# Optimization experiments

Measured on AMD Instinct MI355X. Metric: run time of the kernel, lower is better.

The kernel has to match this reference:

```python
import jax, jax.numpy as jnp
import numpy as np


def _gru(x, Wih, Whh, bih, bhh):
    # single-layer torch-style GRU; x: [B,T,D] -> [B,T,H]
    H = Whh.shape[1]
    gi_all = jnp.einsum('btd,gd->btg', x, Wih) + bih  # [B,T,3H], input gates precomputed

    def step(h, gi):
        gh = h @ Whh.T + bhh
        ir, iz, inn = jnp.split(gi, 3, axis=-1)
        hr, hz, hn = jnp.split(gh, 3, axis=-1)
        r = jax.nn.sigmoid(ir + hr)
        zg = jax.nn.sigmoid(iz + hz)
        n = jnp.tanh(inn + r * hn)
        h_new = (1.0 - zg) * n + zg * h
        return h_new, h_new

    h0 = jnp.zeros((x.shape[0], H), x.dtype)
    _, hs = jax.lax.scan(step, h0, jnp.swapaxes(gi_all, 0, 1))
    return jnp.swapaxes(hs, 0, 1)


def _post(h, W1, b1, W2, b2):
    h = jax.nn.leaky_relu(h @ W1.T + b1, 0.1)
    return jax.nn.leaky_relu(h @ W2.T + b2, 0.1)


def setup_inputs() -> dict:
    B, T, X, Z, H, L = 512, 100, 38, 3, 500, 20
    key = jax.random.key(0)
    ks = iter(jax.random.split(key, 40))
    r = lambda shape, s=0.05: jax.random.normal(next(ks), shape, jnp.float32) * s
    return {
        'x': jax.random.normal(next(ks), (B, T, X), jnp.float32),
        'eps': jax.random.normal(next(ks), (B, T, Z), jnp.float32),
        'enc_Wih': r((3 * H, X)), 'enc_Whh': r((3 * H, H)), 'enc_bih': r((3 * H,)), 'enc_bhh': r((3 * H,)),
        'enc_W1': r((H, H)), 'enc_b1': r((H,)), 'enc_W2': r((H, H)), 'enc_b2': r((H,)),
        'zm_W': r((Z, H + Z)), 'zm_b': r((Z,)), 'zs_W': r((Z, H + Z)), 'zs_b': r((Z,)),
        'flow_w': r((L, Z), 0.5), 'flow_b': r((L,), 0.5), 'flow_u': r((L, Z), 0.5),
        'dec_Wih': r((3 * H, Z)), 'dec_Whh': r((3 * H, H)), 'dec_bih': r((3 * H,)), 'dec_bhh': r((3 * H,)),
        'dec_W1': r((H, H)), 'dec_b1': r((H,)), 'dec_W2': r((H, H)), 'dec_b2': r((H,)),
        'xm_W': r((X, H)), 'xm_b': r((X,)), 'xs_W': r((X, H)), 'xs_b': r((X,)),
    }


def reference(x, eps, enc_Wih, enc_Whh, enc_bih, enc_bhh, enc_W1, enc_b1, enc_W2, enc_b2,
              zm_W, zm_b, zs_W, zs_b, flow_w, flow_b, flow_u,
              dec_Wih, dec_Whh, dec_bih, dec_bhh, dec_W1, dec_b1, dec_W2, dec_b2,
              xm_W, xm_b, xs_W, xs_b):
    # ---- Encoder ----
    h = _gru(x, enc_Wih, enc_Whh, enc_bih, enc_bhh)
    h = _post(h, enc_W1, enc_b1, enc_W2, enc_b2)

    def lat_step(z_prev, inputs):
        ht, et = inputs
        inp = jnp.concatenate([ht, z_prev], axis=-1)
        mu = inp @ zm_W.T + zm_b
        std = jax.nn.softplus(inp @ zs_W.T + zs_b) + 1e-4
        zt = mu + std * et
        return zt, (zt, mu, std)

    z0 = jnp.zeros((x.shape[0], zm_W.shape[0]), x.dtype)
    _, (z_gen, z_mu, z_std) = jax.lax.scan(
        lat_step, z0, (jnp.swapaxes(h, 0, 1), jnp.swapaxes(eps, 0, 1)))
    z_gen = jnp.swapaxes(z_gen, 0, 1)
    z_mu = jnp.swapaxes(z_mu, 0, 1)
    z_std = jnp.swapaxes(z_std, 0, 1)

    # ---- Planar flow stack ----
    def flow_step(carry, p):
        z, ld = carry
        w, b, u = p
        wu = jnp.sum(w * u)
        m = -1.0 + jax.nn.softplus(wu)
        u_hat = u + (m - wu) * w / (jnp.sum(w * w) + 1e-7)
        lin = jnp.sum(z * w, axis=-1, keepdims=True) + b  # [B,T,1]
        t = jnp.tanh(lin)
        fz = z + u_hat * t
        det = 1.0 + (1.0 - t * t) * jnp.sum(u_hat * w)  # sum(u_hat*psi)
        ld = ld + jnp.log(jnp.abs(det) + 1e-7)
        return (fz, ld), None

    ld0 = jnp.zeros(z_gen.shape[:-1] + (1,), z_gen.dtype)
    (z_fin, log_det_jac), _ = jax.lax.scan(flow_step, (z_gen, ld0), (flow_w, flow_b, flow_u))

    # ---- Decoder ----
    hd = _gru(z_fin, dec_Wih, dec_Whh, dec_bih, dec_bhh)
    hd = _post(hd, dec_W1, dec_b1, dec_W2, dec_b2)
    x_rec_mu = hd @ xm_W.T + xm_b
    x_rec_std = jax.nn.softplus(hd @ xs_W.T + xs_b) + 1e-4
    return (x_rec_mu, x_rec_std, z_gen, z_fin, z_mu, z_std, log_det_jac)
```

## Files before the change

### kernel.cpp

```cpp
#include <hip/hip_runtime.h>

typedef unsigned short u16;
typedef unsigned int u32;
typedef unsigned long long u64;
typedef __bf16 bf16x8 __attribute__((ext_vector_type(8)));
typedef float f32x4 __attribute__((ext_vector_type(4)));
typedef u16 u16x8 __attribute__((ext_vector_type(8)));
typedef u16 u16x4 __attribute__((ext_vector_type(4)));
typedef u32 u32x4 __attribute__((ext_vector_type(4)));

#define MFMA16x16(a,b,c) __builtin_amdgcn_mfma_f32_16x16x32_bf16((a),(b),(c),0,0,0)

static __device__ __forceinline__ u16 f2bf(float f){
  u32 u = __builtin_bit_cast(u32, f);
  u += 0x7fffu + ((u >> 16) & 1u);
  return (u16)(u >> 16);
}
static __device__ __forceinline__ float bf2f(u16 h){
  u32 u = ((u32)h) << 16;
  return __builtin_bit_cast(float, u);
}
static __device__ __forceinline__ float fast_sigmoid(float x){
  return 1.f / (1.f + __expf(-x));
}
static __device__ __forceinline__ float fast_tanh(float x){
  float e = __expf(2.f * x);
  return 1.f - 2.f / (e + 1.f);
}
static __device__ __forceinline__ float fast_softplus(float x){
  return (x > 15.f) ? x : __logf(1.f + __expf(x));
}
static __device__ __forceinline__ f32x4 zero4(){
  f32x4 v; v[0]=0.f; v[1]=0.f; v[2]=0.f; v[3]=0.f; return v;
}
static __device__ __forceinline__ f32x4 splat4(float x){
  f32x4 v; v[0]=x; v[1]=x; v[2]=x; v[3]=x; return v;
}

static __device__ __forceinline__ void build_one(
    u16* __restrict__ dst, int mode, int NT, int idx,
    const float* __restrict__ W0, const float* __restrict__ b0,
    const float* __restrict__ W1, const float* __restrict__ b1)
{
  int j    = idx & 7;
  int lane = (idx >> 3) & 63;
  int ntks = idx >> 9;
  int nt   = ntks % NT;
  int ks   = ntks / NT;
  int k    = ks * 32 + ((lane >> 4) << 3) + j;
  int ncol = (nt << 4) + (lane & 15);
  float v = 0.f;
  if (mode == 0){
    int g = ncol >> 9;
    int jin = ncol & 511;
    if (jin < 500){
      int row = g * 500 + jin;
      if (k < 500) v = W0[row * 500 + k];
      else if (k == 511) v = b0[row];
    }
  } else if (mode == 2){
    if (ncol < 500){
      if (k < 500) v = W0[ncol * 500 + k];
      else if (k == 511) v = b0[ncol];
    }
  } else if (mode == 3){
    int c = ncol;
    if (c < 3){
      if (k < 500) v = W0[c * 503 + k];
      else if (k == 511) v = b0[c];
    } else if (c < 6){
      int cc = c - 3;
      if (k < 500) v = W1[cc * 503 + k];
      else if (k == 511) v = b1[cc];
    }
  } else if (mode == 4){
    int grp = ncol / 48;
    int cc  = ncol - grp * 48;
    if (grp < 2 && cc < 38){
      const float* W  = grp ? W1 : W0;
      const float* bb = grp ? b1 : b0;
      if (k < 500) v = W[cc * 500 + k];
      else if (k == 511) v = bb[cc];
    }
  } else {
    int g = ncol >> 9;
    int jin = ncol & 511;
    if (jin < 500 && k < 38) v = W0[(g * 500 + jin) * 38 + k];
  }
  dst[idx] = f2bf(v);
}

__global__ void build_all(
    u16* ENCF, u16* DECF, u16* EGIF, u16* PF0, u16* PF1, u16* PF2, u16* PF3,
    u16* ZFR, u16* HFR, float* FPP, u32* CNT,
    const float* enc_Whh, const float* enc_bhh, const float* enc_Wih,
    const float* dec_Whh, const float* dec_bhh,
    const float* enc_W1, const float* enc_b1, const float* enc_W2, const float* enc_b2,
    const float* dec_W1, const float* dec_b1, const float* dec_W2, const float* dec_b2,
    const float* zm_W, const float* zm_b, const float* zs_W, const float* zs_b,
    const float* xm_W, const float* xm_b, const float* xs_W, const float* xs_b,
    const float* flow_w, const float* flow_b, const float* flow_u)
{
  const int b = blockIdx.x, tid = threadIdx.x;
  if      (b < 3072)  build_one(ENCF,0,96,(b       )*256+tid, enc_Whh,enc_bhh,0,0);
  else if (b < 6144)  build_one(DECF,0,96,(b- 3072 )*256+tid, dec_Whh,dec_bhh,0,0);
  else if (b < 6528)  build_one(EGIF,5,96,(b- 6144 )*256+tid, enc_Wih,0,0,0);
  else if (b < 7552)  build_one(PF0 ,2,32,(b- 6528 )*256+tid, enc_W1,enc_b1,0,0);
  else if (b < 8576)  build_one(PF1 ,2,32,(b- 7552 )*256+tid, enc_W2,enc_b2,0,0);
  else if (b < 9600)  build_one(PF2 ,2,32,(b- 8576 )*256+tid, dec_W1,dec_b1,0,0);
  else if (b < 10624) build_one(PF3 ,2,32,(b- 9600 )*256+tid, dec_W2,dec_b2,0,0);
  else if (b < 10656) build_one(ZFR ,3, 1,(b-10624 )*256+tid, zm_W,zm_b,zs_W,zs_b);
  else if (b < 10848) build_one(HFR ,4, 6,(b-10656 )*256+tid, xm_W,xm_b,xs_W,xs_b);
  else if (b == 10848){
    if (tid < 20){
      int l = tid;
      float w0 = flow_w[l*3+0], w1 = flow_w[l*3+1], w2 = flow_w[l*3+2];
      float u0 = flow_u[l*3+0], u1 = flow_u[l*3+1], u2 = flow_u[l*3+2];
      float wu = w0*u0 + w1*u1 + w2*u2;
      float m  = -1.f + fast_softplus(wu);
      float ww = w0*w0 + w1*w1 + w2*w2 + 1e-7f;
      float sc = (m - wu) / ww;
      float uh0 = u0 + sc*w0, uh1 = u1 + sc*w1, uh2 = u2 + sc*w2;
      float uw  = uh0*w0 + uh1*w1 + uh2*w2;
      FPP[l*8+0]=w0; FPP[l*8+1]=w1; FPP[l*8+2]=w2; FPP[l*8+3]=flow_b[l];
      FPP[l*8+4]=uh0; FPP[l*8+5]=uh1; FPP[l*8+6]=uh2; FPP[l*8+7]=uw;
    }
  } else {
    for (int i = tid; i < 8192; i += 256) CNT[i] = 0;
  }
}

__global__ __launch_bounds__(256, 1) void gru8_kernel(
    const u16* __restrict__ frag, const u16* __restrict__ giw,
    const float* __restrict__ xsrc, const u64* __restrict__ zsrc,
    const float* __restrict__ Wih3, const float* __restrict__ bih3,
    u32* __restrict__ hbufbase, u16* __restrict__ hout, u32* __restrict__ cntbase)
{
  __shared__ u32 hstage[20800];
  __shared__ u16 xstage[1280];
  const int tid  = threadIdx.x, lane = tid & 63;
  const int wv   = tid >> 6;
  const int q    = lane >> 4, c = lane & 15;
  const int gid  = blockIdx.x & 31, s = blockIdx.x >> 5;
  const int b0   = gid * 16;
  const int nt0  = s*4 + wv;
  const int col  = nt0*16 + c;
  u32* cnt = cntbase + gid * 128;
  u32* hb  = hbufbase + (size_t)gid * 8192;
  const bool enc = (giw != nullptr);

  u16x8 wf[3][16];
  #pragma unroll
  for (int ks = 0; ks < 16; ++ks)
    #pragma unroll
    for (int g = 0; g < 3; ++g)
      wf[g][ks] = *(const u16x8*)(frag + (((size_t)ks*96 + g*32 + nt0)*64 + lane)*8);

  u16x8 wih[2][3];
  float bs0 = 0.f, bs1 = 0.f, bs2 = 0.f;
  int xr0=0, xk0=0, xr1=0, xk1=0, xr2=0, xk2=0;
  if (enc){
    #pragma unroll
    for (int ks = 0; ks < 2; ++ks)
      #pragma unroll
      for (int g = 0; g < 3; ++g)
        wih[ks][g] = *(const u16x8*)(giw + (((size_t)ks*96 + g*32 + nt0)*64 + lane)*8);
    if (col < 500){
      bs0 = bih3[col]; bs1 = bih3[500 + col]; bs2 = bih3[1000 + col];
    }
    xr0 = tid / 38;         xk0 = tid - xr0*38;
    int e1 = tid + 256;     xr1 = e1 / 38; xk1 = e1 - xr1*38;
    if (tid < 96){ int e2 = tid + 512; xr2 = e2 / 38; xk2 = e2 - xr2*38; }
  }

  float wz[3][3] = {{0,0,0},{0,0,0},{0,0,0}}, wb[3] = {0,0,0};
  if (!enc && col < 500){
    #pragma unroll
    for (int g = 0; g < 3; ++g){
      #pragma unroll
      for (int k = 0; k < 3; ++k) wz[g][k] = Wih3[(g*500 + col)*3 + k];
      wb[g] = bih3[g*500 + col];
    }
  }

  const int srow = tid >> 4;
  const int spos = (tid & 15) * 2;

  float hold[4] = {0.f, 0.f, 0.f, 0.f};
  u64 zv[4];
  float xf0 = 0.f, xf1 = 0.f, xf2 = 0.f;
  {
    u32 me = (col == 511) ? 0x3F80u : 0u;
    u32 pr = __shfl_xor(me, 1, 64);
    if (!(c & 1)){
      u32 val = me | (pr << 16);
      #pragma unroll
      for (int r = 0; r < 4; ++r){
        hstage[(q*4+r)*260 + (col>>1)] = val;
        __hip_atomic_store(hb + (q*4+r)*256 + (col>>1), val,
                           __ATOMIC_RELAXED, __HIP_MEMORY_SCOPE_AGENT);
      }
    }
    if (enc){
      if (tid < 64){
        int slot = tid >> 5, r = tid & 15, p = (tid >> 4) & 1;
        xstage[slot*640 + r*40 + 38 + p] = 0;
      }
      float v0 = xsrc[((size_t)(b0 + xr0)*100 + 0)*38 + xk0];
      float v1 = xsrc[((size_t)(b0 + xr1)*100 + 0)*38 + xk1];
      xstage[xr0*40 + xk0] = f2bf(v0);
      xstage[xr1*40 + xk1] = f2bf(v1);
      if (tid < 96){
        float v2 = xsrc[((size_t)(b0 + xr2)*100 + 0)*38 + xk2];
        xstage[xr2*40 + xk2] = f2bf(v2);
      }
    } else {
      #pragma unroll
      for (int r = 0; r < 4; ++r)
        zv[r] = zsrc[(size_t)(b0 + q*4 + r)*100 + 0];
    }
  }
  __syncthreads();
  if (tid == 0)
    __hip_atomic_fetch_add(cnt, 1u, __ATOMIC_RELAXED, __HIP_MEMORY_SCOPE_AGENT);

  #pragma unroll 1
  for (int t = 0; t < 100; ++t){
    if (tid == 0){
      const u32 target = 8u*(u32)(t+1);
      int guard = 0;
      while (__hip_atomic_load(cnt, __ATOMIC_RELAXED, __HIP_MEMORY_SCOPE_AGENT) < target){
        if (++guard > (1<<24)) break;
      }
    }
    __syncthreads();

    {
      const u64* src = (const u64*)(hb + (t & 1)*4096);
      u64 sv[7];
      #pragma unroll
      for (int r = 0; r < 7; ++r){
        const int rs = (s + 1 + r) & 7;
        sv[r] = __hip_atomic_load(src + srow*128 + rs*16 + (tid & 15),
                                  __ATOMIC_RELAXED, __HIP_MEMORY_SCOPE_AGENT);
      }
      if (enc && t < 99){
        xf0 = xsrc[((size_t)(b0 + xr0)*100 + (t+1))*38 + xk0];
        xf1 = xsrc[((size_t)(b0 + xr1)*100 + (t+1))*38 + xk1];
        if (tid < 96) xf2 = xsrc[((size_t)(b0 + xr2)*100 + (t+1))*38 + xk2];
      }
      #pragma unroll
      for (int r = 0; r < 7; ++r){
        const int rs = (s + 1 + r) & 7;
        *(u64*)&hstage[srow*260 + rs*32 + spos] = sv[r];
      }
    }
    __syncthreads();

    f32x4 acc0, acc1, acc2, gN;
    if (enc){
      const int slot = t & 1;
      bf16x8 ax0 = *(const bf16x8*)&xstage[slot*640 + c*40 + q*8];
      u16x8 z8 = {0,0,0,0,0,0,0,0};
      bf16x8 ax1 = __builtin_bit_cast(bf16x8, z8);
      if (q == 0) ax1 = *(const bf16x8*)&xstage[slot*640 + c*40 + 32];
      acc0 = splat4(bs0);
      acc0 = MFMA16x16(ax0, __builtin_bit_cast(bf16x8, wih[0][0]), acc0);
      acc0 = MFMA16x16(ax1, __builtin_bit_cast(bf16x8, wih[1][0]), acc0);
      acc1 = splat4(bs1);
      acc1 = MFMA16x16(ax0, __builtin_bit_cast(bf16x8, wih[0][1]), acc1);
      acc1 = MFMA16x16(ax1, __builtin_bit_cast(bf16x8, wih[1][1]), acc1);
      gN   = splat4(bs2);
      gN   = MFMA16x16(ax0, __builtin_bit_cast(bf16x8, wih[0][2]), gN);
      gN   = MFMA16x16(ax1, __builtin_bit_cast(bf16x8, wih[1][2]), gN);
      acc2 = zero4();
    } else {
      acc0 = zero4(); acc1 = zero4(); acc2 = zero4(); gN = zero4();
    }
    #pragma unroll
    for (int ks = 0; ks < 16; ++ks){
      bf16x8 af = *(const bf16x8*)&hstage[c*260 + ks*16 + q*4];
      acc0 = MFMA16x16(af, __builtin_bit_cast(bf16x8, wf[0][ks]), acc0);
      acc1 = MFMA16x16(af, __builtin_bit_cast(bf16x8, wf[1][ks]), acc1);
      acc2 = MFMA16x16(af, __builtin_bit_cast(bf16x8, wf[2][ks]), acc2);
    }
    __syncthreads();

    if (enc && t < 99){
      const int ns = (t+1) & 1;
      xstage[ns*640 + xr0*40 + xk0] = f2bf(xf0);
      xstage[ns*640 + xr1*40 + xk1] = f2bf(xf1);
      if (tid < 96) xstage[ns*640 + xr2*40 + xk2] = f2bf(xf2);
    }

    u16 hvv[4];
    u32* nxt = hb + ((t+1) & 1)*4096;
    {
      #pragma unroll
      for (int r = 0; r < 4; ++r){
        float ar, az, gn;
        if (enc){
          ar = acc0[r]; az = acc1[r]; gn = gN[r];
        } else {
          float z0 = bf2f((u16)(zv[r]));
          float z1 = bf2f((u16)(zv[r] >> 16));
          float z2 = bf2f((u16)(zv[r] >> 32));
          ar = acc0[r] + z0*wz[0][0] + z1*wz[0][1] + z2*wz[0][2] + wb[0];
          az = acc1[r] + z0*wz[1][0] + z1*wz[1][1] + z2*wz[1][2] + wb[1];
          gn = z0*wz[2][0] + z1*wz[2][1] + z2*wz[2][2] + wb[2];
        }
        float an = acc2[r];
        float rr = fast_sigmoid(ar);
        float zz = fast_sigmoid(az);
        float nn = fast_tanh(gn + rr*an);
        float h  = (1.f - zz)*nn + zz*hold[r];
        hold[r] = h;
        u16 hv16 = (col < 500) ? f2bf(h) : ((col == 511) ? (u16)0x3F80 : (u16)0);
        hvv[r] = hv16;
        u32 me = hv16;
        u32 pr = __shfl_xor(me, 1, 64);
        if (!(c & 1)){
          u32 val = me | (pr << 16);
          hstage[(q*4+r)*260 + (col>>1)] = val;
          __hip_atomic_store(nxt + (q*4+r)*256 + (col>>1), val,
                             __ATOMIC_RELAXED, __HIP_MEMORY_SCOPE_AGENT);
        }
      }
    }
    __syncthreads();
    if (tid == 0)
      __hip_atomic_fetch_add(cnt, 1u, __ATOMIC_RELAXED, __HIP_MEMORY_SCOPE_AGENT);
    #pragma unroll
    for (int r = 0; r < 4; ++r)
      __builtin_nontemporal_store(hvv[r],
          hout + ((size_t)(b0 + q*4 + r)*100 + t)*512 + col);
    if (!enc && t < 99){
      #pragma unroll
      for (int r = 0; r < 4; ++r)
        zv[r] = zsrc[(size_t)(b0 + q*4 + r)*100 + (t+1)];
    }
  }
}

__global__ __launch_bounds__(512, 4) void post_chain(
    const u16* __restrict__ A, const u16* __restrict__ fA,
    const u16* __restrict__ fB, const u16* __restrict__ f3,
    float* __restrict__ o0, float* __restrict__ o1, int mode)
{
  __shared__ u16 AS[32768];
  const int tid = threadIdx.x, lane = tid & 63, w = tid >> 6;
  const int q = lane >> 4, c = lane & 15;
  const size_t rowbase = (size_t)blockIdx.x * 64;

  f32x4 acc[4][4];
  #pragma unroll
  for (int rt = 0; rt < 4; ++rt)
    #pragma unroll
    for (int i = 0; i < 4; ++i) acc[rt][i] = zero4();
  #pragma unroll 1
  for (int ks = 0; ks < 16; ++ks){
    bf16x8 bfr[4];
    #pragma unroll
    for (int i = 0; i < 4; ++i){
      const int nt = w*4 + i;
      bfr[i] = __builtin_bit_cast(bf16x8,
          *(const u16x8*)(fA + (((size_t)ks * 32 + nt) * 64 + lane) * 8));
    }
    #pragma unroll
    for (int rt = 0; rt < 4; ++rt){
      bf16x8 af = __builtin_bit_cast(bf16x8,
          *(const u16x8*)(A + (rowbase + rt*16 + c) * 512 + ks * 32 + q * 8));
      #pragma unroll
      for (int i = 0; i < 4; ++i)
        acc[rt][i] = MFMA16x16(af, bfr[i], acc[rt][i]);
    }
  }
  #pragma unroll
  for (int rt = 0; rt < 4; ++rt)
    #pragma unroll
    for (int i = 0; i < 4; ++i){
      const int cl = (w*4 + i)*16 + c;
      const int ks2 = cl >> 5, qq = (cl >> 3) & 3, j = cl & 7;
      #pragma unroll
      for (int r = 0; r < 4; ++r){
        const int m = q*4 + r;
        float v = acc[rt][i][r];
        v = fmaxf(v, 0.1f * v);
        AS[(((rt*16 + ks2)*4 + qq)*16 + m)*8 + j] =
            (cl < 500) ? f2bf(v) : ((cl == 511) ? (u16)0x3F80 : (u16)0);
      }
    }
  __syncthreads();

  #pragma unroll
  for (int rt = 0; rt < 4; ++rt)
    #pragma unroll
    for (int i = 0; i < 4; ++i) acc[rt][i] = zero4();
  #pragma unroll 1
  for (int ks = 0; ks < 16; ++ks){
    bf16x8 bfr[4];
    #pragma unroll
    for (int i = 0; i < 4; ++i){
      const int nt = w*4 + i;
      bfr[i] = __builtin_bit_cast(bf16x8,
          *(const u16x8*)(fB + (((size_t)ks * 32 + nt) * 64 + lane) * 8));
    }
    #pragma unroll
    for (int rt = 0; rt < 4; ++rt){
      bf16x8 af = __builtin_bit_cast(bf16x8,
          *(const u16x8*)&AS[(((rt*16 + ks)*4 + q)*16 + c)*8]);
      #pragma unroll
      for (int i = 0; i < 4; ++i)
        acc[rt][i] = MFMA16x16(af, bfr[i], acc[rt][i]);
    }
  }
  __syncthreads();
  #pragma unroll
  for (int rt = 0; rt < 4; ++rt)
    #pragma unroll
    for (int i = 0; i < 4; ++i){
      const int cl = (w*4 + i)*16 + c;
      const int ks2 = cl >> 5, qq = (cl >> 3) & 3, j = cl & 7;
      #pragma unroll
      for (int r = 0; r < 4; ++r){
        const int m = q*4 + r;
        float v = acc[rt][i][r];
        v = fmaxf(v, 0.1f * v);
        AS[(((rt*16 + ks2)*4 + qq)*16 + m)*8 + j] =
            (cl < 500) ? f2bf(v) : ((cl == 511) ? (u16)0x3F80 : (u16)0);
      }
    }
  __syncthreads();

  if (mode == 0){
    if (w < 4){
      const int rt3 = w;
      f32x4 a3 = zero4();
      #pragma unroll 1
      for (int ks = 0; ks < 16; ++ks){
        bf16x8 af = __builtin_bit_cast(bf16x8,
            *(const u16x8*)&AS[(((rt3*16 + ks)*4 + q)*16 + c)*8]);
        bf16x8 bf = __builtin_bit_cast(bf16x8,
            *(const u16x8*)(f3 + (((size_t)ks * 64) + lane) * 8));
        a3 = MFMA16x16(af, bf, a3);
      }
      if (c < 6){
        #pragma unroll
        for (int r = 0; r < 4; ++r){
          const size_t row = rowbase + rt3*16 + q*4 + r;
          const int tt = (int)(row % 100);
          const int bb = (int)(row / 100);
          o0[((size_t)tt*512 + bb)*8 + c] = a3[r];
        }
      }
    }
  } else {
    const int rt3 = w & 3, hh = w >> 2;
    f32x4 a3[3];
    #pragma unroll
    for (int ii = 0; ii < 3; ++ii) a3[ii] = zero4();
    #pragma unroll 1
    for (int ks = 0; ks < 16; ++ks){
      bf16x8 af = __builtin_bit_cast(bf16x8,
          *(const u16x8*)&AS[(((rt3*16 + ks)*4 + q)*16 + c)*8]);
      #pragma unroll
      for (int ii = 0; ii < 3; ++ii){
        const int nt = hh*3 + ii;
        bf16x8 bf = __builtin_bit_cast(bf16x8,
            *(const u16x8*)(f3 + (((size_t)ks * 6 + nt) * 64 + lane) * 8));
        a3[ii] = MFMA16x16(af, bf, a3[ii]);
      }
    }
    #pragma unroll
    for (int ii = 0; ii < 3; ++ii){
      const int cc = (hh*3 + ii)*16 + c;
      const int grp = cc / 48;
      const int cl = cc - grp * 48;
      if (cl < 38){
        #pragma unroll
        for (int r = 0; r < 4; ++r){
          const size_t row = rowbase + rt3*16 + q*4 + r;
          if (grp == 0) o0[row*38 + cl] = a3[ii][r];
          else          o1[row*38 + cl] = fast_softplus(a3[ii][r]) + 1e-4f;
        }
      }
    }
  }
}

__global__ void scan_kernel(const float* __restrict__ hmT, const float* __restrict__ eps,
                            const float* __restrict__ zmW, const float* __restrict__ zsW,
                            float* __restrict__ zgen, float* __restrict__ zmu,
                            float* __restrict__ zstd)
{
  int b = blockIdx.x * blockDim.x + threadIdx.x;
  if (b >= 512) return;
  float Wm[3][3], Ws[3][3];
  #pragma unroll
  for (int j = 0; j < 3; ++j)
    #pragma unroll
    for (int k = 0; k < 3; ++k){
      Wm[j][k] = zmW[j * 503 + 500 + k];
      Ws[j][k] = zsW[j * 503 + 500 + k];
    }
  f32x4 hA0, hA1, hB0, hB1;
  float eA0, eA1, eA2, eB0, eB1, eB2;
  hA0 = *(const f32x4*)(hmT + ((size_t)0*512 + b)*8);
  hA1 = *(const f32x4*)(hmT + ((size_t)0*512 + b)*8 + 4);
  hB0 = *(const f32x4*)(hmT + ((size_t)1*512 + b)*8);
  hB1 = *(const f32x4*)(hmT + ((size_t)1*512 + b)*8 + 4);
  {
    const float* e0p = eps + ((size_t)b*100 + 0)*3;
    const float* e1p = eps + ((size_t)b*100 + 1)*3;
    eA0 = e0p[0]; eA1 = e0p[1]; eA2 = e0p[2];
    eB0 = e1p[0]; eB1 = e1p[1]; eB2 = e1p[2];
  }
  float z0 = 0.f, z1 = 0.f, z2 = 0.f;
  #pragma unroll 1
  for (int t = 0; t < 100; t += 2){
    {
      float h0 = hA0[0], h1 = hA0[1], h2 = hA0[2];
      float h3 = hA0[3], h4 = hA1[0], h5 = hA1[1];
      float e0 = eA0, e1 = eA1, e2 = eA2;
      if (t + 2 < 100){
        hA0 = *(const f32x4*)(hmT + ((size_t)(t+2)*512 + b)*8);
        hA1 = *(const f32x4*)(hmT + ((size_t)(t+2)*512 + b)*8 + 4);
        const float* ep = eps + ((size_t)b*100 + (t+2))*3;
        eA0 = ep[0]; eA1 = ep[1]; eA2 = ep[2];
      }
      size_t row = (size_t)b*100 + t;
      float m0 = h0 + Wm[0][0]*z0 + Wm[0][1]*z1 + Wm[0][2]*z2;
      float m1 = h1 + Wm[1][0]*z0 + Wm[1][1]*z1 + Wm[1][2]*z2;
      float m2 = h2 + Wm[2][0]*z0 + Wm[2][1]*z1 + Wm[2][2]*z2;
      float s0 = fast_softplus(h3 + Ws[0][0]*z0 + Ws[0][1]*z1 + Ws[0][2]*z2) + 1e-4f;
      float s1 = fast_softplus(h4 + Ws[1][0]*z0 + Ws[1][1]*z1 + Ws[1][2]*z2) + 1e-4f;
      float s2 = fast_softplus(h5 + Ws[2][0]*z0 + Ws[2][1]*z1 + Ws[2][2]*z2) + 1e-4f;
      z0 = m0 + s0*e0; z1 = m1 + s1*e1; z2 = m2 + s2*e2;
      __builtin_nontemporal_store(z0, zgen + row*3 + 0);
      __builtin_nontemporal_store(z1, zgen + row*3 + 1);
      __builtin_nontemporal_store(z2, zgen + row*3 + 2);
      __builtin_nontemporal_store(m0, zmu  + row*3 + 0);
      __builtin_nontemporal_store(m1, zmu  + row*3 + 1);
      __builtin_nontemporal_store(m2, zmu  + row*3 + 2);
      __builtin_nontemporal_store(s0, zstd + row*3 + 0);
      __builtin_nontemporal_store(s1, zstd + row*3 + 1);
      __builtin_nontemporal_store(s2, zstd + row*3 + 2);
    }
    {
      float h0 = hB0[0], h1 = hB0[1], h2 = hB0[2];
      float h3 = hB0[3], h4 = hB1[0], h5 = hB1[1];
      float e0 = eB0, e1 = eB1, e2 = eB2;
      if (t + 3 < 100){
        hB0 = *(const f32x4*)(hmT + ((size_t)(t+3)*512 + b)*8);
        hB1 = *(const f32x4*)(hmT + ((size_t)(t+3)*512 + b)*8 + 4);
        const float* ep = eps + ((size_t)b*100 + (t+3))*3;
        eB0 = ep[0]; eB1 = ep[1]; eB2 = ep[2];
      }
      size_t row = (size_t)b*100 + t + 1;
      float m0 = h0 + Wm[0][0]*z0 + Wm[0][1]*z1 + Wm[0][2]*z2;
      float m1 = h1 + Wm[1][0]*z0 + Wm[1][1]*z1 + Wm[1][2]*z2;
      float m2 = h2 + Wm[2][0]*z0 + Wm[2][1]*z1 + Wm[2][2]*z2;
      float s0 = fast_softplus(h3 + Ws[0][0]*z0 + Ws[0][1]*z1 + Ws[0][2]*z2) + 1e-4f;
      float s1 = fast_softplus(h4 + Ws[1][0]*z0 + Ws[1][1]*z1 + Ws[1][2]*z2) + 1e-4f;
      float s2 = fast_softplus(h5 + Ws[2][0]*z0 + Ws[2][1]*z1 + Ws[2][2]*z2) + 1e-4f;
      z0 = m0 + s0*e0; z1 = m1 + s1*e1; z2 = m2 + s2*e2;
      __builtin_nontemporal_store(z0, zgen + row*3 + 0);
      __builtin_nontemporal_store(z1, zgen + row*3 + 1);
      __builtin_nontemporal_store(z2, zgen + row*3 + 2);
      __builtin_nontemporal_store(m0, zmu  + row*3 + 0);
      __builtin_nontemporal_store(m1, zmu  + row*3 + 1);
      __builtin_nontemporal_store(m2, zmu  + row*3 + 2);
      __builtin_nontemporal_store(s0, zstd + row*3 + 0);
      __builtin_nontemporal_store(s1, zstd + row*3 + 1);
      __builtin_nontemporal_store(s2, zstd + row*3 + 2);
    }
  }
}

__global__ void flow_kernel(const float* __restrict__ zgen, const float* __restrict__ fp,
                            float* __restrict__ zfin, float* __restrict__ ldj,
                            u16* __restrict__ zf16)
{
  int idx = blockIdx.x * blockDim.x + threadIdx.x;
  if (idx >= 51200) return;
  float z0 = zgen[idx*3+0], z1 = zgen[idx*3+1], z2 = zgen[idx*3+2];
  float ld = 0.f;
  #pragma unroll 1
  for (int l = 0; l < 20; ++l){
    const float* p = fp + l * 8;
    float lin = z0*p[0] + z1*p[1] + z2*p[2] + p[3];
    float tt = fast_tanh(lin);
    z0 += p[4]*tt; z1 += p[5]*tt; z2 += p[6]*tt;
    float det = 1.f + (1.f - tt*tt) * p[7];
    ld += __logf(fabsf(det) + 1e-7f);
  }
  zfin[idx*3+0] = z0; zfin[idx*3+1] = z1; zfin[idx*3+2] = z2;
  ldj[idx] = ld;
  u16x4 o; o[0] = f2bf(z0); o[1] = f2bf(z1); o[2] = f2bf(z2); o[3] = 0x3F80;
  *(u16x4*)(zf16 + (size_t)idx * 4) = o;
}

extern "C" void kernel_launch(void* const* d_in, const int* in_sizes, int n_in,
                              void* d_out, int out_size, void* d_ws, size_t ws_size,
                              hipStream_t stream)
{
  const float* x       = (const float*)d_in[0];
  const float* eps     = (const float*)d_in[1];
  const float* enc_Wih = (const float*)d_in[2];
  const float* enc_Whh = (const float*)d_in[3];
  const float* enc_bih = (const float*)d_in[4];
  const float* enc_bhh = (const float*)d_in[5];
  const float* enc_W1  = (const float*)d_in[6];
  const float* enc_b1  = (const float*)d_in[7];
  const float* enc_W2  = (const float*)d_in[8];
  const float* enc_b2  = (const float*)d_in[9];
  const float* zm_W    = (const float*)d_in[10];
  const float* zm_b    = (const float*)d_in[11];
  const float* zs_W    = (const float*)d_in[12];
  const float* zs_b    = (const float*)d_in[13];
  const float* flow_w  = (const float*)d_in[14];
  const float* flow_b  = (const float*)d_in[15];
  const float* flow_u  = (const float*)d_in[16];
  const float* dec_Wih = (const float*)d_in[17];
  const float* dec_Whh = (const float*)d_in[18];
  const float* dec_bih = (const float*)d_in[19];
  const float* dec_bhh = (const float*)d_in[20];
  const float* dec_W1  = (const float*)d_in[21];
  const float* dec_b1  = (const float*)d_in[22];
  const float* dec_W2  = (const float*)d_in[23];
  const float* dec_b2  = (const float*)d_in[24];
  const float* xm_W    = (const float*)d_in[25];
  const float* xm_b    = (const float*)d_in[26];
  const float* xs_W    = (const float*)d_in[27];
  const float* xs_b    = (const float*)d_in[28];
  (void)in_sizes; (void)n_in; (void)out_size; (void)ws_size;

  float* out    = (float*)d_out;
  float* r_mu   = out;
  float* r_std  = out + 1945600;
  float* r_zgen = out + 3891200;
  float* r_zfin = out + 4044800;
  float* r_zmu  = out + 4198400;
  float* r_zstd = out + 4352000;
  float* r_ldj  = out + 4505600;

  char* ws = (char*)d_ws;
  size_t off = 0;
  auto alloc = [&](size_t bytes)->char*{
    char* p = ws + off;
    off += (bytes + 255) & ~(size_t)255;
    return p;
  };
  u16* H1    = (u16*)alloc((size_t)51200*512*2);
  u16* ENCF  = (u16*)alloc((size_t)16*96*512*2);
  u16* DECF  = (u16*)alloc((size_t)16*96*512*2);
  u16* EGIF  = (u16*)alloc((size_t)2*96*512*2);
  u16* PF0   = (u16*)alloc((size_t)16*32*512*2);
  u16* PF1   = (u16*)alloc((size_t)16*32*512*2);
  u16* PF2   = (u16*)alloc((size_t)16*32*512*2);
  u16* PF3   = (u16*)alloc((size_t)16*32*512*2);
  u16* ZFR   = (u16*)alloc((size_t)16*1*512*2);
  u16* HFR   = (u16*)alloc((size_t)16*6*512*2);
  float* FPP = (float*)alloc((size_t)20*8*4);
  float* HM  = (float*)alloc((size_t)51200*8*4);
  u16* ZF16  = (u16*)alloc((size_t)51200*4*2);
  u32* HBUF  = (u32*)alloc((size_t)32*2*16*512*2);
  u32* CNT   = (u32*)alloc((size_t)2*32*128*4);

  build_all<<<10850,256,0,stream>>>(ENCF,DECF,EGIF,PF0,PF1,PF2,PF3,ZFR,HFR,FPP,CNT,
      enc_Whh,enc_bhh,enc_Wih,dec_Whh,dec_bhh,
      enc_W1,enc_b1,enc_W2,enc_b2,dec_W1,dec_b1,dec_W2,dec_b2,
      zm_W,zm_b,zs_W,zs_b,xm_W,xm_b,xs_W,xs_b,flow_w,flow_b,flow_u);

  gru8_kernel<<<256,256,0,stream>>>(ENCF, EGIF, x, nullptr, nullptr, enc_bih,
                                    HBUF, H1, CNT);
  post_chain<<<800,512,0,stream>>>(H1, PF0, PF1, ZFR, HM, nullptr, 0);

  scan_kernel<<<2,256,0,stream>>>(HM, eps, zm_W, zs_W, r_zgen, r_zmu, r_zstd);
  flow_kernel<<<200,256,0,stream>>>(r_zgen, FPP, r_zfin, r_ldj, ZF16);

  gru8_kernel<<<256,256,0,stream>>>(DECF, nullptr, nullptr, (const u64*)ZF16,
                                    dec_Wih, dec_bih, HBUF, H1, CNT + 32*128);
  post_chain<<<800,512,0,stream>>>(H1, PF2, PF3, HFR, r_mu, r_std, 1);
}
```

Before: 1.035 ms.

## Split GRU recurrent K-reduction across two wave halves with LDS partial-sum combine

Doubles the GRU block to 512 threads and splits the 16-step K loop of the recurrent matmul between two wave groups, each holding half the Whh fragments. The upper half also computes the input-gate MFMAs and writes its partial accumulators to shared memory, where the lower half adds them before applying the gate nonlinearities. The goal is a shorter per-timestep critical path on the serial recurrence and fewer weight registers per wave. The cost is an extra LDS round trip and two waves per SIMD competing for issue slots, and all waves still wait at every barrier.

Result: slower. 1.138 ms (+9.9%).

```diff
diff --git a/kernel.cpp b/kernel.cpp
--- a/kernel.cpp
+++ b/kernel.cpp
@@ -130,7 +130,7 @@
   }
 }
 
-__global__ __launch_bounds__(256, 1) void gru8_kernel(
+__global__ __launch_bounds__(512, 2) void gru8_kernel(
     const u16* __restrict__ frag, const u16* __restrict__ giw,
     const float* __restrict__ xsrc, const u64* __restrict__ zsrc,
     const float* __restrict__ Wih3, const float* __restrict__ bih3,
@@ -138,28 +138,32 @@
 {
   __shared__ u32 hstage[20800];
   __shared__ u16 xstage[1280];
+  __shared__ f32x4 pacc[4][64][4];
   const int tid  = threadIdx.x, lane = tid & 63;
-  const int wv   = tid >> 6;
+  const int wv8  = tid >> 6;
+  const int half = wv8 & 1;
+  const int wq   = wv8 >> 1;
   const int q    = lane >> 4, c = lane & 15;
   const int gid  = blockIdx.x & 31, s = blockIdx.x >> 5;
   const int b0   = gid * 16;
-  const int nt0  = s*4 + wv;
+  const int nt0  = s*4 + wq;
   const int col  = nt0*16 + c;
   u32* cnt = cntbase + gid * 128;
   u32* hb  = hbufbase + (size_t)gid * 8192;
   const bool enc = (giw != nullptr);
 
-  u16x8 wf[3][16];
+  u16x8 wf[3][8];
   #pragma unroll
-  for (int ks = 0; ks < 16; ++ks)
+  for (int ksl = 0; ksl < 8; ++ksl){
+    const int ks = half*8 + ksl;
     #pragma unroll
     for (int g = 0; g < 3; ++g)
-      wf[g][ks] = *(const u16x8*)(frag + (((size_t)ks*96 + g*32 + nt0)*64 + lane)*8);
+      wf[g][ksl] = *(const u16x8*)(frag + (((size_t)ks*96 + g*32 + nt0)*64 + lane)*8);
+  }
 
   u16x8 wih[2][3];
   float bs0 = 0.f, bs1 = 0.f, bs2 = 0.f;
-  int xr0=0, xk0=0, xr1=0, xk1=0, xr2=0, xk2=0;
-  if (enc){
+  if (enc && half == 1){
     #pragma unroll
     for (int ks = 0; ks < 2; ++ks)
       #pragma unroll
@@ -168,13 +172,17 @@
     if (col < 500){
       bs0 = bih3[col]; bs1 = bih3[500 + col]; bs2 = bih3[1000 + col];
     }
+  }
+
+  int xr0=0, xk0=0, xr1=0, xk1=0, xr2=0, xk2=0;
+  if (enc && tid < 256){
     xr0 = tid / 38;         xk0 = tid - xr0*38;
     int e1 = tid + 256;     xr1 = e1 / 38; xk1 = e1 - xr1*38;
     if (tid < 96){ int e2 = tid + 512; xr2 = e2 / 38; xk2 = e2 - xr2*38; }
   }
 
   float wz[3][3] = {{0,0,0},{0,0,0},{0,0,0}}, wb[3] = {0,0,0};
-  if (!enc && col < 500){
+  if (!enc && half == 0 && col < 500){
     #pragma unroll
     for (int g = 0; g < 3; ++g){
       #pragma unroll
@@ -190,15 +198,17 @@
   u64 zv[4];
   float xf0 = 0.f, xf1 = 0.f, xf2 = 0.f;
   {
-    u32 me = (col == 511) ? 0x3F80u : 0u;
-    u32 pr = __shfl_xor(me, 1, 64);
-    if (!(c & 1)){
-      u32 val = me | (pr << 16);
-      #pragma unroll
-      for (int r = 0; r < 4; ++r){
-        hstage[(q*4+r)*260 + (col>>1)] = val;
-        __hip_atomic_store(hb + (q*4+r)*256 + (col>>1), val,
-                           __ATOMIC_RELAXED, __HIP_MEMORY_SCOPE_AGENT);
+    if (half == 0){
+      u32 me = (col == 511) ? 0x3F80u : 0u;
+      u32 pr = __shfl_xor(me, 1, 64);
+      if (!(c & 1)){
+        u32 val = me | (pr << 16);
+        #pragma unroll
+        for (int r = 0; r < 4; ++r){
+          hstage[(q*4+r)*260 + (col>>1)] = val;
+          __hip_atomic_store(hb + (q*4+r)*256 + (col>>1), val,
+                             __ATOMIC_RELAXED, __HIP_MEMORY_SCOPE_AGENT);
+        }
       }
     }
     if (enc){
@@ -206,15 +216,17 @@
         int slot = tid >> 5, r = tid & 15, p = (tid >> 4) & 1;
         xstage[slot*640 + r*40 + 38 + p] = 0;
       }
-      float v0 = xsrc[((size_t)(b0 + xr0)*100 + 0)*38 + xk0];
-      float v1 = xsrc[((size_t)(b0 + xr1)*100 + 0)*38 + xk1];
-      xstage[xr0*40 + xk0] = f2bf(v0);
-      xstage[xr1*40 + xk1] = f2bf(v1);
-      if (tid < 96){
-        float v2 = xsrc[((size_t)(b0 + xr2)*100 + 0)*38 + xk2];
-        xstage[xr2*40 + xk2] = f2bf(v2);
-      }
-    } else {
+      if (tid < 256){
+        float v0 = xsrc[((size_t)(b0 + xr0)*100 + 0)*38 + xk0];
+        float v1 = xsrc[((size_t)(b0 + xr1)*100 + 0)*38 + xk1];
+        xstage[xr0*40 + xk0] = f2bf(v0);
+        xstage[xr1*40 + xk1] = f2bf(v1);
+        if (tid < 96){
+          float v2 = xsrc[((size_t)(b0 + xr2)*100 + 0)*38 + xk2];
+          xstage[xr2*40 + xk2] = f2bf(v2);
+        }
+      }
+    } else if (half == 0){
       #pragma unroll
       for (int r = 0; r < 4; ++r)
         zv[r] = zsrc[(size_t)(b0 + q*4 + r)*100 + 0];
@@ -235,7 +247,7 @@
     }
     __syncthreads();
 
-    {
+    if (tid < 256){
       const u64* src = (const u64*)(hb + (t & 1)*4096);
       u64 sv[7];
       #pragma unroll
@@ -258,7 +270,7 @@
     __syncthreads();
 
     f32x4 acc0, acc1, acc2, gN;
-    if (enc){
+    if (enc && half == 1){
       const int slot = t & 1;
       bf16x8 ax0 = *(const bf16x8*)&xstage[slot*640 + c*40 + q*8];
       u16x8 z8 = {0,0,0,0,0,0,0,0};
@@ -278,24 +290,27 @@
       acc0 = zero4(); acc1 = zero4(); acc2 = zero4(); gN = zero4();
     }
     #pragma unroll
-    for (int ks = 0; ks < 16; ++ks){
-      bf16x8 af = *(const bf16x8*)&hstage[c*260 + ks*16 + q*4];
-      acc0 = MFMA16x16(af, __builtin_bit_cast(bf16x8, wf[0][ks]), acc0);
-      acc1 = MFMA16x16(af, __builtin_bit_cast(bf16x8, wf[1][ks]), acc1);
-      acc2 = MFMA16x16(af, __builtin_bit_cast(bf16x8, wf[2][ks]), acc2);
+    for (int ksl = 0; ksl < 8; ++ksl){
+      bf16x8 af = *(const bf16x8*)&hstage[c*260 + (half*8 + ksl)*16 + q*4];
+      acc0 = MFMA16x16(af, __builtin_bit_cast(bf16x8, wf[0][ksl]), acc0);
+      acc1 = MFMA16x16(af, __builtin_bit_cast(bf16x8, wf[1][ksl]), acc1);
+      acc2 = MFMA16x16(af, __builtin_bit_cast(bf16x8, wf[2][ksl]), acc2);
+    }
+    if (half == 1){
+      pacc[wq][lane][0] = acc0;
+      pacc[wq][lane][1] = acc1;
+      pacc[wq][lane][2] = acc2;
+      pacc[wq][lane][3] = gN;
     }
     __syncthreads();
-
-    if (enc && t < 99){
-      const int ns = (t+1) & 1;
-      xstage[ns*640 + xr0*40 + xk0] = f2bf(xf0);
-      xstage[ns*640 + xr1*40 + xk1] = f2bf(xf1);
-      if (tid < 96) xstage[ns*640 + xr2*40 + xk2] = f2bf(xf2);
-    }
 
     u16 hvv[4];
     u32* nxt = hb + ((t+1) & 1)*4096;
-    {
+    if (half == 0){
+      acc0 += pacc[wq][lane][0];
+      acc1 += pacc[wq][lane][1];
+      acc2 += pacc[wq][lane][2];
+      gN   += pacc[wq][lane][3];
       #pragma unroll
       for (int r = 0; r < 4; ++r){
         float ar, az, gn;
@@ -327,17 +342,25 @@
         }
       }
     }
+    if (enc && t < 99 && tid < 256){
+      const int ns = (t+1) & 1;
+      xstage[ns*640 + xr0*40 + xk0] = f2bf(xf0);
+      xstage[ns*640 + xr1*40 + xk1] = f2bf(xf1);
+      if (tid < 96) xstage[ns*640 + xr2*40 + xk2] = f2bf(xf2);
+    }
     __syncthreads();
     if (tid == 0)
       __hip_atomic_fetch_add(cnt, 1u, __ATOMIC_RELAXED, __HIP_MEMORY_SCOPE_AGENT);
-    #pragma unroll
-    for (int r = 0; r < 4; ++r)
-      __builtin_nontemporal_store(hvv[r],
-          hout + ((size_t)(b0 + q*4 + r)*100 + t)*512 + col);
-    if (!enc && t < 99){
+    if (half == 0){
       #pragma unroll
       for (int r = 0; r < 4; ++r)
-        zv[r] = zsrc[(size_t)(b0 + q*4 + r)*100 + (t+1)];
+        __builtin_nontemporal_store(hvv[r],
+            hout + ((size_t)(b0 + q*4 + r)*100 + t)*512 + col);
+      if (!enc && t < 99){
+        #pragma unroll
+        for (int r = 0; r < 4; ++r)
+          zv[r] = zsrc[(size_t)(b0 + q*4 + r)*100 + (t+1)];
+      }
     }
   }
 }
@@ -672,14 +695,14 @@
       enc_W1,enc_b1,enc_W2,enc_b2,dec_W1,dec_b1,dec_W2,dec_b2,
       zm_W,zm_b,zs_W,zs_b,xm_W,xm_b,xs_W,xs_b,flow_w,flow_b,flow_u);
 
-  gru8_kernel<<<256,256,0,stream>>>(ENCF, EGIF, x, nullptr, nullptr, enc_bih,
+  gru8_kernel<<<256,512,0,stream>>>(ENCF, EGIF, x, nullptr, nullptr, enc_bih,
                                     HBUF, H1, CNT);
   post_chain<<<800,512,0,stream>>>(H1, PF0, PF1, ZFR, HM, nullptr, 0);
 
   scan_kernel<<<2,256,0,stream>>>(HM, eps, zm_W, zs_W, r_zgen, r_zmu, r_zstd);
   flow_kernel<<<200,256,0,stream>>>(r_zgen, FPP, r_zfin, r_ldj, ZF16);
 
-  gru8_kernel<<<256,256,0,stream>>>(DECF, nullptr, nullptr, (const u64*)ZF16,
+  gru8_kernel<<<256,512,0,stream>>>(DECF, nullptr, nullptr, (const u64*)ZF16,
                                     dec_Wih, dec_bih, HBUF, H1, CNT + 32*128);
   post_chain<<<800,512,0,stream>>>(H1, PF2, PF3, HFR, r_mu, r_std, 1);
 }
```
